# Performance work log

Hardware: AMD Instinct MI355X
Metric: run time of the kernel (lower is better)

The kernel has to match this reference:

```python
import jax, jax.numpy as jnp
import numpy as np

B, C, H, W = 2, 256, 64, 64
NH, HD, K = 4, 64, 16  # num_head, head_channel, n_clusters
N = H * W
SCALE = HD ** 0.5


def _lin(x, Wm, b):
    return x @ Wm + b


def _mlp(x, W1, b1, W2, b2):
    h = _lin(x, W1, b1)
    h = jnp.where(h > 0, h, 0.01 * h)  # LeakyReLU(0.01)
    return _lin(h, W2, b2)  # dropout p=0.0 -> identity


def setup_inputs() -> dict:
    key = jax.random.key(0)
    ks = jax.random.split(key, 20)
    s = 1.0 / np.sqrt(C)
    s2 = 1.0 / np.sqrt(2 * C)
    inp = {
        "q_img": jax.random.normal(ks[0], (B, C, H, W), jnp.float32),
        "k_img_map": jax.random.normal(ks[1], (B, C, H, W), jnp.float32),
        "v_img_map": jax.random.normal(ks[2], (B, C, H, W), jnp.float32),
        "labels": jax.random.randint(ks[3], (B, H, W), 0, K),
        "pixel_coefficients": jax.random.uniform(ks[4], (B, N, N), jnp.float32),
        "Wq": jax.random.uniform(ks[5], (C, C), jnp.float32, -s, s),
        "bq": jnp.zeros((C,), jnp.float32),
        "Wk": jax.random.uniform(ks[6], (C, C), jnp.float32, -s, s),
        "bk": jnp.zeros((C,), jnp.float32),
        "Wv": jax.random.uniform(ks[7], (C, C), jnp.float32, -s, s),
        "bv": jnp.zeros((C,), jnp.float32),
        "W11": jax.random.uniform(ks[8], (C, 2 * C), jnp.float32, -s, s),
        "b11": jnp.zeros((2 * C,), jnp.float32),
        "W12": jax.random.uniform(ks[9], (2 * C, C), jnp.float32, -s2, s2),
        "b12": jnp.zeros((C,), jnp.float32),
        "W21": jax.random.uniform(ks[10], (C, 2 * C), jnp.float32, -s, s),
        "b21": jnp.zeros((2 * C,), jnp.float32),
        "W22": jax.random.uniform(ks[11], (2 * C, C), jnp.float32, -s2, s2),
        "b22": jnp.zeros((C,), jnp.float32),
    }
    return inp


def reference(q_img, k_img_map, v_img_map, labels, pixel_coefficients,
              Wq, bq, Wk, bk, Wv, bv, W11, b11, W12, b12, W21, b21, W22, b22):
    # [B,C,H,W] -> [B,N,C]
    q = _lin(q_img.transpose(0, 2, 3, 1).reshape(B, N, C), Wq, bq)
    k = _lin(k_img_map.transpose(0, 2, 3, 1).reshape(B, N, C), Wk, bk)
    v = _lin(v_img_map.transpose(0, 2, 3, 1).reshape(B, N, C), Wv, bv)

    lab = labels.reshape(B, N)
    onehot = (lab[:, :, None] == jnp.arange(K)[None, None, :]).astype(jnp.float32)  # [B,N,K]
    num_k = jnp.einsum('bnk,bnc->bkc', onehot, k)
    den_k = onehot.sum(axis=1)[:, :, None] + 1e-6
    centers_k = num_k / den_k  # [B,K,C]

    qm = q.reshape(B, N, NH, HD).transpose(0, 2, 1, 3)  # [B,h,N,d]
    km = k.reshape(B, N, NH, HD).transpose(0, 2, 1, 3)
    vm = v.reshape(B, N, NH, HD).transpose(0, 2, 1, 3)
    cm = centers_k.reshape(B, K, NH, HD).transpose(0, 2, 1, 3)  # [B,h,K,d]

    attn_intra = jnp.einsum('bhnd,bhmd->bhnm', qm, km)          # [B,h,N,N]
    attn_centers = jnp.einsum('bhnd,bhkd->bhnk', qm, cm)        # [B,h,N,K]

    same = (lab[:, :, None] == lab[:, None, :])[:, None]        # [B,1,N,N]
    idx = jnp.broadcast_to(lab[:, None, None, :], (B, NH, N, N))
    attn_inter = jnp.take_along_axis(attn_centers, idx, axis=-1) * pixel_coefficients[:, None]

    scores = jnp.where(same, attn_intra, attn_inter) / SCALE
    attn = jax.nn.softmax(scores, axis=-1)
    out = jnp.einsum('bhnm,bhmd->bhnd', attn, vm).transpose(0, 2, 1, 3).reshape(B, N, C)

    rs1 = v + _mlp(out, W11, b11, W12, b12)        # [B,N,C] (v_spatial residual)
    rs2 = rs1 + _mlp(rs1, W21, b21, W22, b22)
    return rs2.reshape(B, H, W, C).transpose(0, 3, 1, 2)  # [B,C,H,W]
```

## Files before the change

kernel.cpp:

```cpp
#include <hip/hip_runtime.h>
#include <stdint.h>

#define Bv 2
#define Cv 256
#define Nv 4096
#define NHv 4
#define HDv 64
#define Kv 16


typedef __attribute__((ext_vector_type(8))) short bf16x8;
typedef __attribute__((ext_vector_type(4))) float f32x4;

__device__ __forceinline__ float bf2f(unsigned short u) {
  union { unsigned int i; float f; } x; x.i = ((unsigned int)u) << 16; return x.f;
}
__device__ __forceinline__ unsigned short f2bf(float f) {
  union { float f; unsigned int i; } x; x.f = f;
  unsigned int r = x.i + 0x7FFF + ((x.i >> 16) & 1);
  return (unsigned short)(r >> 16);
}
__device__ __forceinline__ unsigned int cvt_pk_bf16(float lo, float hi) {
  unsigned int r;
  asm("v_cvt_pk_bf16_f32 %0, %1, %2" : "=v"(r) : "v"(lo), "v"(hi));
  return r;
}
__device__ __forceinline__ float exp2_raw(float x) {
  float r;
  asm("v_exp_f32 %0, %1" : "=v"(r) : "v"(x));
  return r;
}
__device__ __forceinline__ float bperm_f(int idx_bytes, float v) {
  return __int_as_float(__builtin_amdgcn_ds_bpermute(idx_bytes, __float_as_int(v)));
}

__global__ __launch_bounds__(256) void imgt_k(
    const float* __restrict__ qi, const float* __restrict__ ki,
    const float* __restrict__ vi, unsigned short* __restrict__ dst)
{
  const int z = blockIdx.z;
  const float* src = (z < 2 ? qi : (z < 4 ? ki : vi)) + (long long)(z & 1) * Cv * Nv;
  unsigned short* out = dst + (long long)z * Nv * Cv;
  __shared__ float t[32][33];
  const int x = threadIdx.x, y = threadIdx.y;
  const int n0 = blockIdx.x * 32, c0 = blockIdx.y * 32;
  for (int i = y; i < 32; i += 8)
    t[i][x] = src[(long long)(c0 + i) * Nv + n0 + x];
  __syncthreads();
  for (int i = y; i < 32; i += 8)
    out[(long long)(n0 + i) * Cv + c0 + x] = f2bf(t[x][i]);
}

struct WP { const float* p[7]; };

__global__ __launch_bounds__(256) void wt_k(WP wp, unsigned short* __restrict__ dst)
{
  const int z = blockIdx.z;
  const int KD[7] = {256, 256, 256, 256, 512, 256, 512};
  const int ND[7] = {256, 256, 256, 512, 256, 512, 256};
  const long long OFF[7] = {0, 65536, 131072, 196608, 327680, 458752, 589824};
  const int Kw = KD[z], Nw = ND[z];
  const int nb = blockIdx.x * 32, kb2 = blockIdx.y * 32;
  if (nb >= Nw || kb2 >= Kw) return;
  __shared__ float t[32][33];
  const int x = threadIdx.x, y = threadIdx.y;
  const float* src = wp.p[z];
  for (int i = y; i < 32; i += 8)
    t[i][x] = src[(long long)(kb2 + i) * Nw + nb + x];
  __syncthreads();
  for (int i = y; i < 32; i += 8)
    dst[OFF[z] + (long long)(nb + i) * Kw + kb2 + x] = f2bf(t[x][i]);
}

__global__ __launch_bounds__(256) void proj64_k(
    const unsigned short* __restrict__ imgT, const unsigned short* __restrict__ wt,
    const float* __restrict__ bq, const float* __restrict__ bk, const float* __restrict__ bv,
    unsigned short* __restrict__ qbf, unsigned short* __restrict__ kbf,
    float* __restrict__ vpp, unsigned short* __restrict__ vtb)
{
  __shared__ __align__(16) unsigned short As[64][72];
  __shared__ __align__(16) unsigned short Bs[64][72];
  const int tid = threadIdx.x;
  const int w = tid >> 6, lane = tid & 63;
  const int lr = lane & 15, quad = lane >> 4;
  const int m0 = blockIdx.x * 64, n0 = blockIdx.y * 64;
  const int z = blockIdx.z, zz = z >> 1, bb = z & 1;
  const int wm = (w >> 1) * 32, wn = (w & 1) * 32;
  const int sr = tid >> 2, sh = (tid & 3) * 16;
  const long long NvCv = (long long)Nv * Cv;

  const float* bias = zz == 0 ? bq : (zz == 1 ? bk : bv);
  const unsigned short* Ab0 = imgT + (long long)z * NvCv + (long long)(m0 + sr) * Cv + sh;
  const unsigned short* Bb0 = wt + (long long)zz * 65536 + (long long)(n0 + sr) * Cv + sh;

  f32x4 acc[2][2];
#pragma unroll
  for (int i = 0; i < 2; ++i)
#pragma unroll
    for (int j = 0; j < 2; ++j) acc[i][j] = (f32x4){0.f, 0.f, 0.f, 0.f};

  uint4 rA0 = *(const uint4*)Ab0, rA1 = *(const uint4*)(Ab0 + 8);
  uint4 rB0 = *(const uint4*)Bb0, rB1 = *(const uint4*)(Bb0 + 8);

  for (int k0 = 0; k0 < Cv; k0 += 64) {
    *(uint4*)&As[sr][sh] = rA0; *(uint4*)&As[sr][sh + 8] = rA1;
    *(uint4*)&Bs[sr][sh] = rB0; *(uint4*)&Bs[sr][sh + 8] = rB1;
    __syncthreads();
    if (k0 + 64 < Cv) {
      rA0 = *(const uint4*)(Ab0 + k0 + 64); rA1 = *(const uint4*)(Ab0 + k0 + 72);
      rB0 = *(const uint4*)(Bb0 + k0 + 64); rB1 = *(const uint4*)(Bb0 + k0 + 72);
    }
#pragma unroll
    for (int ks = 0; ks < 2; ++ks) {
      bf16x8 af[2], bfr[2];
#pragma unroll
      for (int i = 0; i < 2; ++i)
        af[i] = *(const bf16x8*)&As[wm + i * 16 + lr][ks * 32 + quad * 8];
#pragma unroll
      for (int j = 0; j < 2; ++j)
        bfr[j] = *(const bf16x8*)&Bs[wn + j * 16 + lr][ks * 32 + quad * 8];
#pragma unroll
      for (int i = 0; i < 2; ++i)
#pragma unroll
        for (int j = 0; j < 2; ++j)
          acc[i][j] = __builtin_amdgcn_mfma_f32_16x16x32_bf16(af[i], bfr[j], acc[i][j], 0, 0, 0);
    }
    __syncthreads();
  }

#pragma unroll
  for (int j = 0; j < 2; ++j) {
    const int col = n0 + wn + j * 16 + lr;
    const float bvv = bias[col];
#pragma unroll
    for (int i = 0; i < 2; ++i) {
      const int mb = m0 + wm + i * 16 + quad * 4;
      float r[4];
#pragma unroll
      for (int reg = 0; reg < 4; ++reg) r[reg] = acc[i][j][reg] + bvv;
      const long long ob = (long long)bb * NvCv;
      if (zz == 0) {
#pragma unroll
        for (int reg = 0; reg < 4; ++reg)
          qbf[ob + (long long)(mb + reg) * Cv + col] = f2bf(r[reg] * 0.18033688f);
      } else if (zz == 1) {
#pragma unroll
        for (int reg = 0; reg < 4; ++reg)
          kbf[ob + (long long)(mb + reg) * Cv + col] = f2bf(r[reg]);
      } else {
#pragma unroll
        for (int reg = 0; reg < 4; ++reg)
          vpp[ob + (long long)(mb + reg) * Cv + col] = r[reg];
        uint2 pk;
        pk.x = cvt_pk_bf16(r[0], r[1]);
        pk.y = cvt_pk_bf16(r[2], r[3]);
        *(uint2*)&vtb[ob + (long long)col * Nv + mb] = pk;
      }
    }
  }
}

template<bool ABF16, int ACT, int RES, int OM>
__global__ __launch_bounds__(256) void mm64_k(
    const void* __restrict__ A, const unsigned short* __restrict__ Bt,
    const float* __restrict__ bias, const float* __restrict__ Res,
    float* __restrict__ outF, unsigned short* __restrict__ outB,
    int M, int Nn, int Kd)
{
  __shared__ __align__(16) unsigned short As[64][72];
  __shared__ __align__(16) unsigned short Bs[64][72];
  const int tid = threadIdx.x;
  const int w = tid >> 6, lane = tid & 63;
  const int lr = lane & 15, quad = lane >> 4;
  const int m0 = blockIdx.x * 64, n0 = blockIdx.y * 64;
  const int wm = (w >> 1) * 32, wn = (w & 1) * 32;
  const int sr = tid >> 2, sh = (tid & 3) * 16;

  f32x4 acc[2][2];
#pragma unroll
  for (int i = 0; i < 2; ++i)
#pragma unroll
    for (int j = 0; j < 2; ++j) acc[i][j] = (f32x4){0.f, 0.f, 0.f, 0.f};

  const long long abase = (long long)(m0 + sr) * Kd + sh;
  const unsigned short* Bb = Bt + (long long)(n0 + sr) * Kd + sh;

  uint4 rA0, rA1, rB0, rB1;
  float4 fA[4];
  if (ABF16) {
    const unsigned short* Ab = (const unsigned short*)A + abase;
    rA0 = *(const uint4*)Ab; rA1 = *(const uint4*)(Ab + 8);
  } else {
    const float* Af = (const float*)A + abase;
    fA[0] = *(const float4*)Af;      fA[1] = *(const float4*)(Af + 4);
    fA[2] = *(const float4*)(Af + 8); fA[3] = *(const float4*)(Af + 12);
  }
  rB0 = *(const uint4*)Bb; rB1 = *(const uint4*)(Bb + 8);

  for (int k0 = 0; k0 < Kd; k0 += 64) {
    if (ABF16) {
      *(uint4*)&As[sr][sh] = rA0; *(uint4*)&As[sr][sh + 8] = rA1;
    } else {
#pragma unroll
      for (int t = 0; t < 2; ++t) {
        uint4 pk;
        pk.x = cvt_pk_bf16(fA[t * 2].x, fA[t * 2].y);
        pk.y = cvt_pk_bf16(fA[t * 2].z, fA[t * 2].w);
        pk.z = cvt_pk_bf16(fA[t * 2 + 1].x, fA[t * 2 + 1].y);
        pk.w = cvt_pk_bf16(fA[t * 2 + 1].z, fA[t * 2 + 1].w);
        *(uint4*)&As[sr][sh + t * 8] = pk;
      }
    }
    *(uint4*)&Bs[sr][sh] = rB0; *(uint4*)&Bs[sr][sh + 8] = rB1;
    __syncthreads();
    if (k0 + 64 < Kd) {
      if (ABF16) {
        const unsigned short* Ab = (const unsigned short*)A + abase + k0 + 64;
        rA0 = *(const uint4*)Ab; rA1 = *(const uint4*)(Ab + 8);
      } else {
        const float* Af = (const float*)A + abase + k0 + 64;
        fA[0] = *(const float4*)Af;      fA[1] = *(const float4*)(Af + 4);
        fA[2] = *(const float4*)(Af + 8); fA[3] = *(const float4*)(Af + 12);
      }
      rB0 = *(const uint4*)(Bb + k0 + 64); rB1 = *(const uint4*)(Bb + k0 + 72);
    }
#pragma unroll
    for (int ks = 0; ks < 2; ++ks) {
      bf16x8 af[2], bfr[2];
#pragma unroll
      for (int i = 0; i < 2; ++i)
        af[i] = *(const bf16x8*)&As[wm + i * 16 + lr][ks * 32 + quad * 8];
#pragma unroll
      for (int j = 0; j < 2; ++j)
        bfr[j] = *(const bf16x8*)&Bs[wn + j * 16 + lr][ks * 32 + quad * 8];
#pragma unroll
      for (int i = 0; i < 2; ++i)
#pragma unroll
        for (int j = 0; j < 2; ++j)
          acc[i][j] = __builtin_amdgcn_mfma_f32_16x16x32_bf16(af[i], bfr[j], acc[i][j], 0, 0, 0);
    }
    __syncthreads();
  }

#pragma unroll
  for (int j = 0; j < 2; ++j) {
    const int col = n0 + wn + j * 16 + lr;
    const float bv = bias[col];
#pragma unroll
    for (int i = 0; i < 2; ++i) {
      const int mb = m0 + wm + i * 16 + quad * 4;
      float r[4];
#pragma unroll
      for (int reg = 0; reg < 4; ++reg) {
        float v = acc[i][j][reg] + bv;
        if (ACT) v = v > 0.f ? v : 0.01f * v;
        if (RES) v += Res[(long long)(mb + reg) * Nn + col];
        r[reg] = v;
      }
      if (OM == 0) {
#pragma unroll
        for (int reg = 0; reg < 4; ++reg)
          outF[(long long)(mb + reg) * Nn + col] = r[reg];
      } else if (OM == 1) {
#pragma unroll
        for (int reg = 0; reg < 4; ++reg)
          outB[(long long)(mb + reg) * Nn + col] = f2bf(r[reg]);
      } else if (OM == 2) {
#pragma unroll
        for (int reg = 0; reg < 4; ++reg) {
          outF[(long long)(mb + reg) * Nn + col] = r[reg];
          outB[(long long)(mb + reg) * Nn + col] = f2bf(r[reg]);
        }
      } else {
        const float4 st = {r[0], r[1], r[2], r[3]};
        *(float4*)&outF[((long long)((mb >> 12) * Cv + col)) * Nv + (mb & 4095)] = st;
      }
    }
  }
}

__global__ __launch_bounds__(256) void zero_k(float* p, int n)
{
  const int i = blockIdx.x * 256 + threadIdx.x;
  if (i < n) p[i] = 0.f;
}

__global__ __launch_bounds__(256) void center_accum(
    const unsigned short* __restrict__ kb, const int* __restrict__ labels,
    float* __restrict__ cent, float* __restrict__ cnts)
{
  __shared__ int lab_s[512];
  const int bx = blockIdx.x;
  const int chunk = bx & 7;
  const int kk = (bx >> 3) & 15;
  const int b = bx >> 7;
  const int c = threadIdx.x;
  const int nbase = chunk * 512;
  for (int i = threadIdx.x; i < 512; i += 256) lab_s[i] = labels[b * Nv + nbase + i];
  __syncthreads();
  float acc = 0.f;
  int cnt = 0;
#pragma unroll 4
  for (int i = 0; i < 512; ++i) {
    if (lab_s[i] == kk) {
      acc += bf2f(kb[(long long)(b * Nv + nbase + i) * Cv + c]);
      ++cnt;
    }
  }
  atomicAdd(&cent[(b * Kv + kk) * Cv + c], acc);
  if (c == 0) atomicAdd(&cnts[b * Kv + kk], (float)cnt);
}

__global__ __launch_bounds__(256) void center_norm(float* cent, const float* cnts)
{
  const int i = blockIdx.x * 256 + threadIdx.x;
  cent[i] = cent[i] / (cnts[i >> 8] + 1e-6f);
}

union PSCS {
  unsigned short p[4][16][68];
  float c[16][68];
};

__global__ __launch_bounds__(256) void attn_k(
    const unsigned short* __restrict__ qb, const unsigned short* __restrict__ kb,
    const unsigned short* __restrict__ vtb, const float* __restrict__ cent,
    const int* __restrict__ labels, const float* __restrict__ pc,
    float* __restrict__ opart, float* __restrict__ lpart)
{
  __shared__ __align__(16) unsigned short q_s[64][72];
  __shared__ __align__(16) unsigned short k_s[64][72];
  __shared__ __align__(16) unsigned short vt_s[64][72];
  __shared__ __align__(16) PSCS u_s;
  __shared__ float ac_s[64][17];

  const int tid = threadIdx.x;
  const int lane = tid & 63, w = tid >> 6;
  const int lr = lane & 15, quad = lane >> 4;
  const int bx = blockIdx.x;
  const int qt = bx & 63, h = (bx >> 6) & 3, b = (bx >> 8) & 1;
  const int part = bx >> 9;
  const int n0 = qt * 64;
  const int mbase = part * 2048;
  const int sr2 = tid >> 2, so2 = (tid & 3) * 16;
  const int row_l = w * 16 + quad * 4;
  const long long pcb = (long long)b * Nv * Nv;

  {
    const unsigned short* src = qb + ((long long)(b * Nv + n0 + sr2)) * Cv + h * HDv + so2;
    *(uint4*)&q_s[sr2][so2] = *(const uint4*)src;
    *(uint4*)&q_s[sr2][so2 + 8] = *(const uint4*)(src + 8);
  }
  for (int idx = tid; idx < Kv * HDv; idx += 256)
    u_s.c[idx >> 6][idx & 63] = cent[((long long)(b * Kv + (idx >> 6))) * Cv + h * HDv + (idx & 63)];

  uint4 ka0, ka1, va0, va1;
  float pc1[4][4];
  int labm1[4], labq[4];
  {
    const long long ks = ((long long)(b * Nv + mbase + sr2)) * Cv + h * HDv + so2;
    ka0 = *(const uint4*)(kb + ks); ka1 = *(const uint4*)(kb + ks + 8);
    const long long vs = ((long long)(b * Cv + h * HDv + sr2)) * Nv + mbase + so2;
    va0 = *(const uint4*)(vtb + vs); va1 = *(const uint4*)(vtb + vs + 8);
  }
#pragma unroll
  for (int sub = 0; sub < 4; ++sub) {
    labm1[sub] = labels[b * Nv + mbase + sub * 16 + lr];
#pragma unroll
    for (int reg = 0; reg < 4; ++reg)
      pc1[sub][reg] = pc[pcb + (long long)(n0 + row_l + reg) * Nv + mbase + sub * 16 + lr];
  }
#pragma unroll
  for (int reg = 0; reg < 4; ++reg) labq[reg] = labels[b * Nv + n0 + row_l + reg];

  __syncthreads();
  for (int idx = tid; idx < 64 * Kv; idx += 256) {
    const int r = idx >> 4, kk = idx & 15;
    float s = 0.f;
#pragma unroll
    for (int d = 0; d < HDv; ++d) s += bf2f(q_s[r][d]) * u_s.c[kk][d];
    ac_s[r][kk] = s;
  }
  const bf16x8 qa0 = *(const bf16x8*)&q_s[w * 16 + lr][quad * 8];
  const bf16x8 qa1 = *(const bf16x8*)&q_s[w * 16 + lr][32 + quad * 8];
  __syncthreads();

  float acv[4];
#pragma unroll
  for (int reg = 0; reg < 4; ++reg) acv[reg] = ac_s[w * 16 + quad * 4 + reg][lr];

  float acg[4][4];
#pragma unroll
  for (int sub = 0; sub < 4; ++sub) {
    const int bidx = (quad << 6) + (labm1[sub] << 2);
#pragma unroll
    for (int reg = 0; reg < 4; ++reg)
      acg[sub][reg] = bperm_f(bidx, acv[reg]);
  }

  *(uint4*)&k_s[sr2][so2] = ka0; *(uint4*)&k_s[sr2][so2 + 8] = ka1;
  *(uint4*)&vt_s[sr2][so2] = va0; *(uint4*)&vt_s[sr2][so2 + 8] = va1;
  __syncthreads();

  f32x4 oacc[4];
#pragma unroll
  for (int s2 = 0; s2 < 4; ++s2) oacc[s2] = (f32x4){0.f, 0.f, 0.f, 0.f};
  float lrow[4] = {0.f, 0.f, 0.f, 0.f};

  for (int t = 0; t < 32; ++t) {
    const int m0 = mbase + t * 64;
    const bool has = (t < 31);

    if (has) {
      const long long ks = ((long long)(b * Nv + m0 + 64 + sr2)) * Cv + h * HDv + so2;
      ka0 = *(const uint4*)(kb + ks); ka1 = *(const uint4*)(kb + ks + 8);
      const long long vs = ((long long)(b * Cv + h * HDv + sr2)) * Nv + m0 + 64 + so2;
      va0 = *(const uint4*)(vtb + vs); va1 = *(const uint4*)(vtb + vs + 8);
    }

    f32x4 sacc[4];
    __builtin_amdgcn_s_setprio(1);
#pragma unroll
    for (int sub = 0; sub < 4; ++sub) {
      const bf16x8 kb0 = *(const bf16x8*)&k_s[sub * 16 + lr][quad * 8];
      const bf16x8 kb1 = *(const bf16x8*)&k_s[sub * 16 + lr][32 + quad * 8];
      f32x4 s = (f32x4){0.f, 0.f, 0.f, 0.f};
      s = __builtin_amdgcn_mfma_f32_16x16x32_bf16(qa0, kb0, s, 0, 0, 0);
      s = __builtin_amdgcn_mfma_f32_16x16x32_bf16(qa1, kb1, s, 0, 0, 0);
      sacc[sub] = s;
    }
    __builtin_amdgcn_s_setprio(0);

#pragma unroll
    for (int sub = 0; sub < 4; ++sub) {
      float p4[4];
#pragma unroll
      for (int reg = 0; reg < 4; ++reg) {
        const float s = (labm1[sub] == labq[reg]) ? sacc[sub][reg]
                                                  : acg[sub][reg] * pc1[sub][reg];
        const float p = exp2_raw(s);
        lrow[reg] += p;
        p4[reg] = p;
      }
      const unsigned int pk01 = cvt_pk_bf16(p4[0], p4[1]);
      const unsigned int pk23 = cvt_pk_bf16(p4[2], p4[3]);
      unsigned short* pp = &u_s.p[w][quad * 4][sub * 16 + lr];
      pp[0]   = (unsigned short)pk01;
      pp[68]  = (unsigned short)(pk01 >> 16);
      pp[136] = (unsigned short)pk23;
      pp[204] = (unsigned short)(pk23 >> 16);
    }

    if (has) {
#pragma unroll
      for (int sub = 0; sub < 4; ++sub) {
        labm1[sub] = labels[b * Nv + m0 + 64 + sub * 16 + lr];
#pragma unroll
        for (int reg = 0; reg < 4; ++reg)
          pc1[sub][reg] = pc[pcb + (long long)(n0 + row_l + reg) * Nv + m0 + 64 + sub * 16 + lr];
      }
    }

    const bf16x8 pa0 = *(const bf16x8*)&u_s.p[w][lr][quad * 8];
    const bf16x8 pa1 = *(const bf16x8*)&u_s.p[w][lr][32 + quad * 8];
    __builtin_amdgcn_s_setprio(1);
#pragma unroll
    for (int sub = 0; sub < 4; ++sub) {
      const bf16x8 vb0 = *(const bf16x8*)&vt_s[sub * 16 + lr][quad * 8];
      const bf16x8 vb1 = *(const bf16x8*)&vt_s[sub * 16 + lr][32 + quad * 8];
      oacc[sub] = __builtin_amdgcn_mfma_f32_16x16x32_bf16(pa0, vb0, oacc[sub], 0, 0, 0);
      oacc[sub] = __builtin_amdgcn_mfma_f32_16x16x32_bf16(pa1, vb1, oacc[sub], 0, 0, 0);
    }
    __builtin_amdgcn_s_setprio(0);

    if (has) {
#pragma unroll
      for (int sub = 0; sub < 4; ++sub) {
        const int bidx = (quad << 6) + (labm1[sub] << 2);
#pragma unroll
        for (int reg = 0; reg < 4; ++reg)
          acg[sub][reg] = bperm_f(bidx, acv[reg]);
      }
    }

    __syncthreads();
    if (has) {
      *(uint4*)&k_s[sr2][so2] = ka0; *(uint4*)&k_s[sr2][so2 + 8] = ka1;
      *(uint4*)&vt_s[sr2][so2] = va0; *(uint4*)&vt_s[sr2][so2 + 8] = va1;
    }
    __syncthreads();
  }

#pragma unroll
  for (int reg = 0; reg < 4; ++reg) {
    float l = lrow[reg];
    l += __shfl_xor(l, 1); l += __shfl_xor(l, 2);
    l += __shfl_xor(l, 4); l += __shfl_xor(l, 8);
    const int row = n0 + row_l + reg;
    const long long obase = (long long)part * 2097152 + ((long long)(b * Nv + row)) * Cv + h * HDv;
#pragma unroll
    for (int sub = 0; sub < 4; ++sub)
      opart[obase + sub * 16 + lr] = oacc[sub][reg];
    if (lr == 0)
      lpart[part * 32768 + (b * 4 + h) * 4096 + row] = l;
  }
}

__global__ __launch_bounds__(256) void combine_k(
    const float* __restrict__ op, const float* __restrict__ lp,
    unsigned short* __restrict__ aob)
{
  const long long i4 = ((long long)blockIdx.x * 256 + threadIdx.x) * 4;
  const int c = (int)(i4 & 255), n = (int)((i4 >> 8) & 4095), b = (int)(i4 >> 20);
  const int h = c >> 6;
  const float l = lp[(b * 4 + h) * 4096 + n] + lp[32768 + (b * 4 + h) * 4096 + n];
  const float inv = 1.f / l;
  const float4 a = *(const float4*)&op[i4];
  const float4 d = *(const float4*)&op[2097152 + i4];
  uint2 pk;
  pk.x = cvt_pk_bf16((a.x + d.x) * inv, (a.y + d.y) * inv);
  pk.y = cvt_pk_bf16((a.z + d.z) * inv, (a.w + d.w) * inv);
  *(uint2*)&aob[i4] = pk;
}

extern "C" void kernel_launch(void* const* d_in, const int* in_sizes, int n_in,
                              void* d_out, int out_size, void* d_ws, size_t ws_size,
                              hipStream_t stream)
{
  const float* q_img = (const float*)d_in[0];
  const float* k_img = (const float*)d_in[1];
  const float* v_img = (const float*)d_in[2];
  const int* labels  = (const int*)d_in[3];
  const float* pc    = (const float*)d_in[4];
  const float* Wq  = (const float*)d_in[5];  const float* bq  = (const float*)d_in[6];
  const float* Wk  = (const float*)d_in[7];  const float* bk  = (const float*)d_in[8];
  const float* Wv  = (const float*)d_in[9];  const float* bv  = (const float*)d_in[10];
  const float* W11 = (const float*)d_in[11]; const float* b11 = (const float*)d_in[12];
  const float* W12 = (const float*)d_in[13]; const float* b12 = (const float*)d_in[14];
  const float* W21 = (const float*)d_in[15]; const float* b21 = (const float*)d_in[16];
  const float* W22 = (const float*)d_in[17]; const float* b22 = (const float*)d_in[18];
  float* outp = (float*)d_out;

  const long long SZ = (long long)Bv * Nv * Cv;
  float* ws    = (float*)d_ws;
  float* vpp   = ws;
  float* rs1   = vpp + SZ;
  float* opart = rs1 + SZ;
  float* lpart = opart + 2 * SZ;
  float* cent  = lpart + 65536;
  float* cnts  = cent + Bv * Kv * Cv;
  unsigned short* wt   = (unsigned short*)(cnts + Bv * Kv);
  unsigned short* qbf  = wt + 720896;
  unsigned short* kbf  = qbf + SZ;
  unsigned short* vtb  = kbf + SZ;
  unsigned short* aob  = vtb + SZ;
  unsigned short* h1b  = aob + SZ;
  unsigned short* imgT = aob;

  imgt_k<<<dim3(Nv / 32, Cv / 32, 6), dim3(32, 8), 0, stream>>>(q_img, k_img, v_img, imgT);
  WP wp = {{Wq, Wk, Wv, W11, W12, W21, W22}};
  wt_k<<<dim3(16, 16, 7), dim3(32, 8), 0, stream>>>(wp, wt);

  proj64_k<<<dim3(64, 4, 6), 256, 0, stream>>>(imgT, wt, bq, bk, bv, qbf, kbf, vpp, vtb);

  zero_k<<<dim3(33), 256, 0, stream>>>(cent, Bv * Kv * Cv + Bv * Kv);
  center_accum<<<dim3(Bv * Kv * 8), 256, 0, stream>>>(kbf, labels, cent, cnts);
  center_norm<<<dim3(Bv * Kv * Cv / 256), 256, 0, stream>>>(cent, cnts);

  attn_k<<<dim3(1024), 256, 0, stream>>>(qbf, kbf, vtb, cent, labels, pc, opart, lpart);
  combine_k<<<dim3(2048), 256, 0, stream>>>(opart, lpart, aob);

  mm64_k<true, 1, 0, 1><<<dim3(128, 8), 256, 0, stream>>>(
      aob, wt + 196608, b11, nullptr, nullptr, h1b, 2 * Nv, 2 * Cv, Cv);
  mm64_k<true, 0, 1, 2><<<dim3(128, 4), 256, 0, stream>>>(
      h1b, wt + 327680, b12, vpp, rs1, aob, 2 * Nv, Cv, 2 * Cv);

  mm64_k<true, 1, 0, 1><<<dim3(128, 8), 256, 0, stream>>>(
      aob, wt + 458752, b21, nullptr, nullptr, h1b, 2 * Nv, 2 * Cv, Cv);
  mm64_k<true, 0, 1, 4><<<dim3(128, 4), 256, 0, stream>>>(
      h1b, wt + 589824, b22, rs1, outp, nullptr, 2 * Nv, Cv, 2 * Cv);
}
```

Baseline: 403.6 us.

## Fuse zeroing and center normalization into other kernels; reuse LDS in attention

The zero-fill of the center accumulators moves into an extra z-slice of the weight transpose kernel, and the center normalization now happens inside the attention kernel at load time. Both changes remove separate launches. The attention kernel drops its dedicated LDS union by staging centers in k_s and probabilities in q_s, which cuts shared memory use and may raise occupancy. Cross-lane bpermute gathers of center scores become direct LDS reads from ac_s indexed by label, which may cause bank conflicts.

Measured after the change: 396.2 us. No clear change (-1.8%).

```diff
diff --git a/kernel.cpp b/kernel.cpp
--- a/kernel.cpp
+++ b/kernel.cpp
@@ -29,9 +29,6 @@
   float r;
   asm("v_exp_f32 %0, %1" : "=v"(r) : "v"(x));
   return r;
-}
-__device__ __forceinline__ float bperm_f(int idx_bytes, float v) {
-  return __int_as_float(__builtin_amdgcn_ds_bpermute(idx_bytes, __float_as_int(v)));
 }
 
 __global__ __launch_bounds__(256) void imgt_k(
@@ -53,9 +50,15 @@
 
 struct WP { const float* p[7]; };
 
-__global__ __launch_bounds__(256) void wt_k(WP wp, unsigned short* __restrict__ dst)
+__global__ __launch_bounds__(256) void wt_k(WP wp, unsigned short* __restrict__ dst,
+                                            float* __restrict__ zp, int zn)
 {
   const int z = blockIdx.z;
+  if (z == 7) {
+    const int idx = (blockIdx.y * 16 + blockIdx.x) * 256 + threadIdx.y * 32 + threadIdx.x;
+    if (idx < zn) zp[idx] = 0.f;
+    return;
+  }
   const int KD[7] = {256, 256, 256, 256, 512, 256, 512};
   const int ND[7] = {256, 256, 256, 512, 256, 512, 256};
   const long long OFF[7] = {0, 65536, 131072, 196608, 327680, 458752, 589824};
@@ -277,12 +280,6 @@
       }
     }
   }
-}
-
-__global__ __launch_bounds__(256) void zero_k(float* p, int n)
-{
-  const int i = blockIdx.x * 256 + threadIdx.x;
-  if (i < n) p[i] = 0.f;
 }
 
 __global__ __launch_bounds__(256) void center_accum(
@@ -311,27 +308,15 @@
   if (c == 0) atomicAdd(&cnts[b * Kv + kk], (float)cnt);
 }
 
-__global__ __launch_bounds__(256) void center_norm(float* cent, const float* cnts)
-{
-  const int i = blockIdx.x * 256 + threadIdx.x;
-  cent[i] = cent[i] / (cnts[i >> 8] + 1e-6f);
-}
-
-union PSCS {
-  unsigned short p[4][16][68];
-  float c[16][68];
-};
-
 __global__ __launch_bounds__(256) void attn_k(
     const unsigned short* __restrict__ qb, const unsigned short* __restrict__ kb,
     const unsigned short* __restrict__ vtb, const float* __restrict__ cent,
-    const int* __restrict__ labels, const float* __restrict__ pc,
-    float* __restrict__ opart, float* __restrict__ lpart)
+    const float* __restrict__ cnts, const int* __restrict__ labels,
+    const float* __restrict__ pc, float* __restrict__ opart, float* __restrict__ lpart)
 {
   __shared__ __align__(16) unsigned short q_s[64][72];
   __shared__ __align__(16) unsigned short k_s[64][72];
   __shared__ __align__(16) unsigned short vt_s[64][72];
-  __shared__ __align__(16) PSCS u_s;
   __shared__ float ac_s[64][17];
 
   const int tid = threadIdx.x;
@@ -351,8 +336,12 @@
     *(uint4*)&q_s[sr2][so2] = *(const uint4*)src;
     *(uint4*)&q_s[sr2][so2 + 8] = *(const uint4*)(src + 8);
   }
-  for (int idx = tid; idx < Kv * HDv; idx += 256)
-    u_s.c[idx >> 6][idx & 63] = cent[((long long)(b * Kv + (idx >> 6))) * Cv + h * HDv + (idx & 63)];
+  float* c_s = (float*)&k_s[0][0];
+  for (int idx = tid; idx < Kv * HDv; idx += 256) {
+    const int kk = idx >> 6, d = idx & 63;
+    c_s[kk * 68 + d] = cent[((long long)(b * Kv + kk)) * Cv + h * HDv + d]
+                       / (cnts[b * Kv + kk] + 1e-6f);
+  }
 
   uint4 ka0, ka1, va0, va1;
   float pc1[4][4];
@@ -378,25 +367,19 @@
     const int r = idx >> 4, kk = idx & 15;
     float s = 0.f;
 #pragma unroll
-    for (int d = 0; d < HDv; ++d) s += bf2f(q_s[r][d]) * u_s.c[kk][d];
+    for (int d = 0; d < HDv; ++d) s += bf2f(q_s[r][d]) * c_s[kk * 68 + d];
     ac_s[r][kk] = s;
   }
   const bf16x8 qa0 = *(const bf16x8*)&q_s[w * 16 + lr][quad * 8];
   const bf16x8 qa1 = *(const bf16x8*)&q_s[w * 16 + lr][32 + quad * 8];
   __syncthreads();
 
-  float acv[4];
-#pragma unroll
-  for (int reg = 0; reg < 4; ++reg) acv[reg] = ac_s[w * 16 + quad * 4 + reg][lr];
-
   float acg[4][4];
 #pragma unroll
-  for (int sub = 0; sub < 4; ++sub) {
-    const int bidx = (quad << 6) + (labm1[sub] << 2);
+  for (int sub = 0; sub < 4; ++sub)
 #pragma unroll
     for (int reg = 0; reg < 4; ++reg)
-      acg[sub][reg] = bperm_f(bidx, acv[reg]);
-  }
+      acg[sub][reg] = ac_s[row_l + reg][labm1[sub]];
 
   *(uint4*)&k_s[sr2][so2] = ka0; *(uint4*)&k_s[sr2][so2 + 8] = ka1;
   *(uint4*)&vt_s[sr2][so2] = va0; *(uint4*)&vt_s[sr2][so2 + 8] = va1;
@@ -444,11 +427,11 @@
       }
       const unsigned int pk01 = cvt_pk_bf16(p4[0], p4[1]);
       const unsigned int pk23 = cvt_pk_bf16(p4[2], p4[3]);
-      unsigned short* pp = &u_s.p[w][quad * 4][sub * 16 + lr];
+      unsigned short* pp = &q_s[w * 16 + quad * 4][sub * 16 + lr];
       pp[0]   = (unsigned short)pk01;
-      pp[68]  = (unsigned short)(pk01 >> 16);
-      pp[136] = (unsigned short)pk23;
-      pp[204] = (unsigned short)(pk23 >> 16);
+      pp[72]  = (unsigned short)(pk01 >> 16);
+      pp[144] = (unsigned short)pk23;
+      pp[216] = (unsigned short)(pk23 >> 16);
     }
 
     if (has) {
@@ -461,8 +444,8 @@
       }
     }
 
-    const bf16x8 pa0 = *(const bf16x8*)&u_s.p[w][lr][quad * 8];
-    const bf16x8 pa1 = *(const bf16x8*)&u_s.p[w][lr][32 + quad * 8];
+    const bf16x8 pa0 = *(const bf16x8*)&q_s[w * 16 + lr][quad * 8];
+    const bf16x8 pa1 = *(const bf16x8*)&q_s[w * 16 + lr][32 + quad * 8];
     __builtin_amdgcn_s_setprio(1);
 #pragma unroll
     for (int sub = 0; sub < 4; ++sub) {
@@ -475,12 +458,10 @@
 
     if (has) {
 #pragma unroll
-      for (int sub = 0; sub < 4; ++sub) {
-        const int bidx = (quad << 6) + (labm1[sub] << 2);
-#pragma unroll
-        for (int reg = 0; reg < 4; ++reg)
-          acg[sub][reg] = bperm_f(bidx, acv[reg]);
-      }
+      for (int sub = 0; sub < 4; ++sub)
+#pragma unroll
+        for (int reg = 0; reg < 4; ++reg)
+          acg[sub][reg] = ac_s[row_l + reg][labm1[sub]];
     }
 
     __syncthreads();
@@ -559,15 +540,13 @@
 
   imgt_k<<<dim3(Nv / 32, Cv / 32, 6), dim3(32, 8), 0, stream>>>(q_img, k_img, v_img, imgT);
   WP wp = {{Wq, Wk, Wv, W11, W12, W21, W22}};
-  wt_k<<<dim3(16, 16, 7), dim3(32, 8), 0, stream>>>(wp, wt);
+  wt_k<<<dim3(16, 16, 8), dim3(32, 8), 0, stream>>>(wp, wt, cent, Bv * Kv * Cv + Bv * Kv);
 
   proj64_k<<<dim3(64, 4, 6), 256, 0, stream>>>(imgT, wt, bq, bk, bv, qbf, kbf, vpp, vtb);
 
-  zero_k<<<dim3(33), 256, 0, stream>>>(cent, Bv * Kv * Cv + Bv * Kv);
   center_accum<<<dim3(Bv * Kv * 8), 256, 0, stream>>>(kbf, labels, cent, cnts);
-  center_norm<<<dim3(Bv * Kv * Cv / 256), 256, 0, stream>>>(cent, cnts);
-
-  attn_k<<<dim3(1024), 256, 0, stream>>>(qbf, kbf, vtb, cent, labels, pc, opart, lpart);
+
+  attn_k<<<dim3(1024), 256, 0, stream>>>(qbf, kbf, vtb, cent, cnts, labels, pc, opart, lpart);
   combine_k<<<dim3(2048), 256, 0, stream>>>(opart, lpart, aob);
 
   mm64_k<true, 1, 0, 1><<<dim3(128, 8), 256, 0, stream>>>(
```
